# Optimization experiments

Measured on AMD Instinct MI355X. Metric: run time of the kernel, lower is better.

Reference implementation:

```python
import jax, jax.numpy as jnp
import numpy as np

NUM_HEADS = 8
AGENT_NUM = 144
POOL_SIZE = 12  # int(sqrt(agent_num))


def _adaptive_pool_matrix(H, out):
    # Row i averages input rows [floor(i*H/out), ceil((i+1)*H/out)) -- PyTorch AdaptiveAvgPool2d semantics.
    P = np.zeros((out, H), dtype=np.float32)
    for i in range(out):
        s = (i * H) // out
        e = -((-(i + 1) * H) // out)
        P[i, s:e] = 1.0 / (e - s)
    return jnp.asarray(P)


def setup_inputs() -> dict:
    key = jax.random.key(0)
    ks = jax.random.split(key, 4)
    b, n, c = 16, 3136, 512
    return {
        "x": jax.random.normal(ks[0], (b, n, c), dtype=jnp.float32),
        "qkv_w": jax.random.normal(ks[1], (3 * c, c), dtype=jnp.float32) * 0.02,
        "proj_w": jax.random.normal(ks[2], (c, c), dtype=jnp.float32) * 0.02,
        "proj_b": jnp.zeros((c,), dtype=jnp.float32),
        "dwc_w": jax.random.normal(ks[3], (c, 1, 3, 3), dtype=jnp.float32) * 0.1,
        "dwc_b": jnp.zeros((c,), dtype=jnp.float32),
    }


def reference(x, qkv_w, proj_w, proj_b, dwc_w, dwc_b):
    b, n, c = x.shape
    H = NUM_HEADS
    d = c // H
    hh = int(n ** 0.5)  # 56
    scale = d ** -0.5

    qkv = x @ qkv_w.T  # (b, n, 3c)
    q, k, v = jnp.split(qkv, 3, axis=-1)

    # adaptive avg pool of q (as b,h,w,c image) down to 12x12 -> agent tokens
    P = _adaptive_pool_matrix(hh, POOL_SIZE)  # (12, 56)
    agent = jnp.einsum('ph,qw,bhwc->bpqc', P, P, q.reshape(b, hh, hh, c))
    agent = agent.reshape(b, AGENT_NUM, c)

    def heads(t):
        return t.reshape(b, -1, H, d).transpose(0, 2, 1, 3)  # (b, H, L, d)

    qh, kh, vh, ah = heads(q), heads(k), heads(v), heads(agent)

    # stage 1: agent-to-key attention
    agent_attn = jax.nn.softmax((ah * scale) @ kh.transpose(0, 1, 3, 2), axis=-1)  # (b,H,144,n)
    agent_v = agent_attn @ vh  # (b,H,144,d)

    # stage 2: query-to-agent attention
    q_attn = jax.nn.softmax((qh * scale) @ ah.transpose(0, 1, 3, 2), axis=-1)  # (b,H,n,144)
    out = (q_attn @ agent_v).transpose(0, 2, 1, 3).reshape(b, n, c)

    # depthwise 3x3 conv residual on v image
    v_img = v.reshape(b, hh, hh, c).transpose(0, 3, 1, 2)  # NCHW
    dw = jax.lax.conv_general_dilated(
        v_img, dwc_w, window_strides=(1, 1), padding='SAME',
        feature_group_count=c, dimension_numbers=('NCHW', 'OIHW', 'NCHW'))
    dw = dw + dwc_b[None, :, None, None]
    out = out + dw.transpose(0, 2, 3, 1).reshape(b, n, c)

    return out @ proj_w.T + proj_b
```

## Files before the change

kernel.cpp:

```cpp
#include <hip/hip_runtime.h>
#include <hip/hip_bf16.h>
#include <math.h>

typedef unsigned short u16;
typedef __attribute__((ext_vector_type(8))) unsigned short u16x8;
typedef __attribute__((ext_vector_type(8))) short bf16x8;
typedef __attribute__((ext_vector_type(4))) float f32x4;

#define BATCH 16
#define NTOK  3136
#define CHN   512
#define NH    8
#define HD    64
#define HHW   56
#define NAG   144
#define PS    12

#define S1PP   72
#define S2PP   152
#define ASP    72
#define AVP    152

__device__ __forceinline__ float b2f(u16 u) {
    unsigned int x = ((unsigned int)u) << 16;
    float f;
    __builtin_memcpy(&f, &x, 4);
    return f;
}
__device__ __forceinline__ u16 f2b(float f) {
    unsigned int x;
    __builtin_memcpy(&x, &f, 4);
    unsigned int lsb = (x >> 16) & 1u;
    x += 0x7fffu + lsb;
    return (u16)(x >> 16);
}
__device__ __forceinline__ void store1(float* p, float v) { *p = v; }
__device__ __forceinline__ void store1(u16* p, float v)   { *p = f2b(v); }

__global__ __launch_bounds__(256) void cvt_f32_bf16_kernel(
    const float* __restrict__ src, u16* __restrict__ dst, int n4)
{
    const int idx = blockIdx.x * 256 + threadIdx.x;
    if (idx >= n4) return;
    float4 v = reinterpret_cast<const float4*>(src)[idx];
    ushort4 o;
    o.x = f2b(v.x); o.y = f2b(v.y); o.z = f2b(v.z); o.w = f2b(v.w);
    reinterpret_cast<ushort4*>(dst)[idx] = o;
}

template <typename OT, bool BIAS>
__global__ __launch_bounds__(256) void mfma_gemm_kernel(
    const u16* __restrict__ A, const u16* __restrict__ W,
    const float* __restrict__ bias, OT* __restrict__ out)
{
    __shared__ u16 Asm[128 * 64];
    __shared__ u16 Bsm[128 * 64];

    const int tid  = threadIdx.x;
    const int lane = tid & 63;
    const int w    = tid >> 6;
    const int m0   = blockIdx.x * 128;
    const int n0   = blockIdx.y * 128;
    const int wm   = (w & 1) * 64;
    const int wn   = (w >> 1) * 64;

    const int srow = lane >> 3;
    const int scol = (lane & 7) * 8;

    f32x4 acc[4][4] = {};

    for (int kt = 0; kt < 8; ++kt) {
        const int k0 = kt * 64;
        __syncthreads();
        #pragma unroll
        for (int i = 0; i < 4; ++i) {
            const int rb = w * 8 + i * 32;
            __builtin_amdgcn_global_load_lds(
                (const __attribute__((address_space(1))) void*)
                    (A + (size_t)(m0 + rb + srow) * 512 + k0 + scol),
                (__attribute__((address_space(3))) void*)(Asm + rb * 64),
                16, 0, 0);
        }
        #pragma unroll
        for (int i = 0; i < 4; ++i) {
            const int rb = w * 8 + i * 32;
            __builtin_amdgcn_global_load_lds(
                (const __attribute__((address_space(1))) void*)
                    (W + (size_t)(n0 + rb + srow) * 512 + k0 + scol),
                (__attribute__((address_space(3))) void*)(Bsm + rb * 64),
                16, 0, 0);
        }
        __syncthreads();

        #pragma unroll
        for (int kh = 0; kh < 2; ++kh) {
            bf16x8 af[4], bfr[4];
            #pragma unroll
            for (int t = 0; t < 4; ++t)
                af[t] = *reinterpret_cast<const bf16x8*>(
                    &Asm[(wm + t * 16 + (lane & 15)) * 64 + kh * 32 + (lane >> 4) * 8]);
            #pragma unroll
            for (int t = 0; t < 4; ++t)
                bfr[t] = *reinterpret_cast<const bf16x8*>(
                    &Bsm[(wn + t * 16 + (lane & 15)) * 64 + kh * 32 + (lane >> 4) * 8]);
            #pragma unroll
            for (int i = 0; i < 4; ++i)
                #pragma unroll
                for (int j = 0; j < 4; ++j)
                    acc[i][j] = __builtin_amdgcn_mfma_f32_16x16x32_bf16(
                        af[i], bfr[j], acc[i][j], 0, 0, 0);
        }
    }

    const int quad = lane >> 4;
    const int col  = lane & 15;
    #pragma unroll
    for (int j = 0; j < 4; ++j) {
        const int n = n0 + wn + j * 16 + col;
        const float bv = BIAS ? bias[n] : 0.f;
        #pragma unroll
        for (int i = 0; i < 4; ++i) {
            #pragma unroll
            for (int r = 0; r < 4; ++r) {
                const int m = m0 + wm + i * 16 + quad * 4 + r;
                store1(&out[(size_t)m * 512 + n], acc[i][j][r] + bv);
            }
        }
    }
}

__global__ __launch_bounds__(256) void pool_x_kernel(
    const float* __restrict__ x, u16* __restrict__ x_pool)
{
    const int b = blockIdx.x, pq = blockIdx.y;
    const int p = pq / PS, qq = pq % PS;
    const int sp_ = (p * HHW) / PS, ep_ = ((p + 1) * HHW + PS - 1) / PS;
    const int sq_ = (qq * HHW) / PS, eq_ = ((qq + 1) * HHW + PS - 1) / PS;
    const float inv = 1.0f / (float)((ep_ - sp_) * (eq_ - sq_));
    for (int ch = threadIdx.x; ch < CHN; ch += 256) {
        float acc = 0.f;
        for (int y = sp_; y < ep_; ++y)
            for (int xx = sq_; xx < eq_; ++xx)
                acc += x[((size_t)b * NTOK + y * HHW + xx) * CHN + ch];
        x_pool[((size_t)b * NAG + pq) * CHN + ch] = f2b(acc * inv);
    }
}

__global__ __launch_bounds__(256) void transpose_v_kernel(
    const u16* __restrict__ v, u16* __restrict__ vt)
{
    __shared__ u16 T[64 * S1PP + 32];
    const int t0 = blockIdx.x * 64;
    const int c0 = blockIdx.y * 64;
    const int b  = blockIdx.z;

    const int r  = threadIdx.x >> 2;
    const int cc = (threadIdx.x & 3) * 16;
    const u16* src = v + ((size_t)b * NTOK + t0 + r) * CHN + c0 + cc;
    u16x8 a0 = *reinterpret_cast<const u16x8*>(src);
    u16x8 a1 = *reinterpret_cast<const u16x8*>(src + 8);
    const int skw = (cc >> 4) * 8;
    #pragma unroll
    for (int j = 0; j < 8; ++j) T[(cc + j) * S1PP + r + skw] = a0[j];
    #pragma unroll
    for (int j = 0; j < 8; ++j) T[(cc + 8 + j) * S1PP + r + skw] = a1[j];
    __syncthreads();

    const int cr  = threadIdx.x >> 2;
    const int tt  = (threadIdx.x & 3) * 16;
    const int rsk = (cr >> 4) * 8;
    u16* dst = vt + ((size_t)b * CHN + c0 + cr) * NTOK + t0 + tt;
    *reinterpret_cast<u16x8*>(dst)     = *reinterpret_cast<const u16x8*>(&T[cr * S1PP + tt + rsk]);
    *reinterpret_cast<u16x8*>(dst + 8) = *reinterpret_cast<const u16x8*>(&T[cr * S1PP + tt + 8 + rsk]);
}

__global__ __launch_bounds__(64) void stage1_mfma_kernel(
    const u16* __restrict__ k, const u16* __restrict__ vt,
    const u16* __restrict__ agent, u16* __restrict__ avt)
{
    __shared__ u16 Pl[16 * S1PP];

    const int lb   = blockIdx.x;
    const int work = (lb & 7) * 144 + (lb >> 3);
    const int at   = work % 9;
    const int r2   = work / 9;
    const int h    = r2 & 7;
    const int b    = r2 >> 3;

    const int lane = threadIdx.x;
    const int c = lane & 15, g = lane >> 4;

    const u16* kp = k  + (size_t)b * NTOK * CHN + h * HD;
    const u16* vp = vt + ((size_t)(b * NH + h)) * HD * NTOK;
    const u16* ap = agent + ((size_t)b * NAG + at * 16 + c) * CHN + h * HD + g * 8;

    bf16x8 af0 = *reinterpret_cast<const bf16x8*>(ap);
    bf16x8 af1 = *reinterpret_cast<const bf16x8*>(ap + 32);

    f32x4 accO[4] = {};
    float m_ = -1e30f, l_ = 0.f;

    bf16x8 kf[8];
    #pragma unroll
    for (int kt = 0; kt < 4; ++kt)
        #pragma unroll
        for (int ks = 0; ks < 2; ++ks)
            kf[kt * 2 + ks] = *reinterpret_cast<const bf16x8*>(
                kp + (size_t)(kt * 16 + c) * CHN + ks * 32 + g * 8);

    for (int key0 = 0; key0 < NTOK; key0 += 64) {
        bf16x8 vf[8];
        #pragma unroll
        for (int dt = 0; dt < 4; ++dt)
            #pragma unroll
            for (int kk = 0; kk < 2; ++kk)
                vf[dt * 2 + kk] = *reinterpret_cast<const bf16x8*>(
                    vp + (size_t)(dt * 16 + c) * NTOK + key0 + kk * 32 + g * 8);
        bf16x8 kn[8];
        const bool more = (key0 + 64) < NTOK;
        if (more) {
            #pragma unroll
            for (int kt = 0; kt < 4; ++kt)
                #pragma unroll
                for (int ks = 0; ks < 2; ++ks)
                    kn[kt * 2 + ks] = *reinterpret_cast<const bf16x8*>(
                        kp + (size_t)(key0 + 64 + kt * 16 + c) * CHN + ks * 32 + g * 8);
        }

        f32x4 s[4] = {};
        #pragma unroll
        for (int kt = 0; kt < 4; ++kt) {
            s[kt] = __builtin_amdgcn_mfma_f32_16x16x32_bf16(kf[kt * 2 + 0], af0, s[kt], 0, 0, 0);
            s[kt] = __builtin_amdgcn_mfma_f32_16x16x32_bf16(kf[kt * 2 + 1], af1, s[kt], 0, 0, 0);
        }

        float tmax = -1e30f;
        #pragma unroll
        for (int kt = 0; kt < 4; ++kt)
            #pragma unroll
            for (int r = 0; r < 4; ++r) tmax = fmaxf(tmax, s[kt][r]);
        tmax = fmaxf(tmax, __shfl_xor(tmax, 16));
        tmax = fmaxf(tmax, __shfl_xor(tmax, 32));

        const float mnew  = fmaxf(m_, tmax * 0.125f);
        const float alpha = __expf(m_ - mnew);
        float psum = 0.f;
        #pragma unroll
        for (int kt = 0; kt < 4; ++kt) {
            float p0 = __expf(s[kt][0] * 0.125f - mnew);
            float p1 = __expf(s[kt][1] * 0.125f - mnew);
            float p2 = __expf(s[kt][2] * 0.125f - mnew);
            float p3 = __expf(s[kt][3] * 0.125f - mnew);
            psum += (p0 + p1) + (p2 + p3);
            ushort4 pk;
            pk.x = f2b(p0); pk.y = f2b(p1); pk.z = f2b(p2); pk.w = f2b(p3);
            *reinterpret_cast<ushort4*>(&Pl[c * S1PP + kt * 16 + g * 4]) = pk;
        }
        psum += __shfl_xor(psum, 16);
        psum += __shfl_xor(psum, 32);
        l_ = l_ * alpha + psum;
        m_ = mnew;
        #pragma unroll
        for (int dt = 0; dt < 4; ++dt) {
            accO[dt][0] *= alpha; accO[dt][1] *= alpha;
            accO[dt][2] *= alpha; accO[dt][3] *= alpha;
        }

        asm volatile("s_waitcnt lgkmcnt(0)" ::: "memory");
        __builtin_amdgcn_sched_barrier(0);

        bf16x8 pf0 = *reinterpret_cast<const bf16x8*>(&Pl[c * S1PP + g * 8]);
        bf16x8 pf1 = *reinterpret_cast<const bf16x8*>(&Pl[c * S1PP + 32 + g * 8]);

        #pragma unroll
        for (int dt = 0; dt < 4; ++dt) {
            accO[dt] = __builtin_amdgcn_mfma_f32_16x16x32_bf16(vf[dt * 2 + 0], pf0, accO[dt], 0, 0, 0);
            accO[dt] = __builtin_amdgcn_mfma_f32_16x16x32_bf16(vf[dt * 2 + 1], pf1, accO[dt], 0, 0, 0);
        }

        if (more) {
            #pragma unroll
            for (int i = 0; i < 8; ++i) kf[i] = kn[i];
        }
    }

    const float invl = 1.f / l_;
    const size_t dbase = (size_t)(b * NH + h) * HD;
    #pragma unroll
    for (int dt = 0; dt < 4; ++dt)
        #pragma unroll
        for (int r = 0; r < 4; ++r)
            avt[(dbase + dt * 16 + g * 4 + r) * NAG + at * 16 + c] =
                f2b(accO[dt][r] * invl);
}

__global__ __launch_bounds__(256, 3) void stage2_mfma_kernel(
    const u16* __restrict__ q,
    const u16* __restrict__ agent,
    const u16* __restrict__ avt,
    const u16* __restrict__ v,
    const float* __restrict__ dwc_w,
    const float* __restrict__ dwc_b,
    u16* __restrict__ xattn)
{
    __shared__ __align__(16) u16 AsPl[NAG * ASP];
    __shared__ __align__(16) u16 AVs[HD * AVP];
    __shared__ float dwW[HD * 9];
    __shared__ float dwB[HD];

    const int h   = blockIdx.y;
    const int b   = blockIdx.z;
    const int tid = threadIdx.x;
    const int w    = tid >> 6;
    const int lane = tid & 63;
    const int c = lane & 15, g = lane >> 4;
    const int q0 = (blockIdx.x * 4 + w) * 16;
    const int qg = q0 + c;
    const int y = qg / HHW, xx = qg % HHW;

    const u16* qp = q + ((size_t)b * NTOK + qg) * CHN + h * HD + g * 8;
    bf16x8 qf0 = *reinterpret_cast<const bf16x8*>(qp);
    bf16x8 qf1 = *reinterpret_cast<const bf16x8*>(qp + 32);

    {
        const u16* ab = agent + (size_t)b * NAG * CHN + h * HD;
        for (int idx = tid; idx < NAG * 4; idx += 256) {
            const int r = idx >> 2, cc = (idx & 3) * 16;
            *reinterpret_cast<u16x8*>(&AsPl[r * ASP + cc]) =
                *reinterpret_cast<const u16x8*>(ab + (size_t)r * CHN + cc);
            *reinterpret_cast<u16x8*>(&AsPl[r * ASP + cc + 8]) =
                *reinterpret_cast<const u16x8*>(ab + (size_t)r * CHN + cc + 8);
        }
        const u16* avb = avt + (size_t)(b * NH + h) * HD * NAG;
        for (int idx = tid; idx < HD * 18; idx += 256) {
            const int r = idx / 18, cc = (idx % 18) * 8;
            *reinterpret_cast<u16x8*>(&AVs[r * AVP + cc]) =
                *reinterpret_cast<const u16x8*>(avb + (size_t)r * NAG + cc);
        }
        for (int idx = tid; idx < HD * 9; idx += 256)
            dwW[idx] = dwc_w[(h * HD + idx / 9) * 9 + (idx % 9)];
        if (tid < HD) dwB[tid] = dwc_b[h * HD + tid];
    }
    __syncthreads();

    float conv[4][4];
    #pragma unroll
    for (int dt = 0; dt < 4; ++dt)
        #pragma unroll
        for (int r = 0; r < 4; ++r) conv[dt][r] = 0.f;
    {
        const u16* vq = v + ((size_t)b * NTOK + qg) * CHN + h * HD + g * 4;
        #pragma unroll
        for (int dy = -1; dy <= 1; ++dy) {
            #pragma unroll
            for (int dx = -1; dx <= 1; ++dx) {
                const int tap = (dy + 1) * 3 + (dx + 1);
                const int yy = y + dy, xc = xx + dx;
                const bool ok = (yy >= 0 && yy < HHW && xc >= 0 && xc < HHW);
                const u16* vr = vq + (ok ? (ptrdiff_t)(dy * HHW + dx) * CHN : 0);
                ushort4 vv0 = *reinterpret_cast<const ushort4*>(vr);
                ushort4 vv1 = *reinterpret_cast<const ushort4*>(vr + 16);
                ushort4 vv2 = *reinterpret_cast<const ushort4*>(vr + 32);
                ushort4 vv3 = *reinterpret_cast<const ushort4*>(vr + 48);
                if (ok) {
                    const float* wt = &dwW[(g * 4) * 9 + tap];
                    conv[0][0] += b2f(vv0.x) * wt[(0 * 16 + 0) * 9];
                    conv[0][1] += b2f(vv0.y) * wt[(0 * 16 + 1) * 9];
                    conv[0][2] += b2f(vv0.z) * wt[(0 * 16 + 2) * 9];
                    conv[0][3] += b2f(vv0.w) * wt[(0 * 16 + 3) * 9];
                    conv[1][0] += b2f(vv1.x) * wt[(1 * 16 + 0) * 9];
                    conv[1][1] += b2f(vv1.y) * wt[(1 * 16 + 1) * 9];
                    conv[1][2] += b2f(vv1.z) * wt[(1 * 16 + 2) * 9];
                    conv[1][3] += b2f(vv1.w) * wt[(1 * 16 + 3) * 9];
                    conv[2][0] += b2f(vv2.x) * wt[(2 * 16 + 0) * 9];
                    conv[2][1] += b2f(vv2.y) * wt[(2 * 16 + 1) * 9];
                    conv[2][2] += b2f(vv2.z) * wt[(2 * 16 + 2) * 9];
                    conv[2][3] += b2f(vv2.w) * wt[(2 * 16 + 3) * 9];
                    conv[3][0] += b2f(vv3.x) * wt[(3 * 16 + 0) * 9];
                    conv[3][1] += b2f(vv3.y) * wt[(3 * 16 + 1) * 9];
                    conv[3][2] += b2f(vv3.z) * wt[(3 * 16 + 2) * 9];
                    conv[3][3] += b2f(vv3.w) * wt[(3 * 16 + 3) * 9];
                }
            }
        }
    }

    f32x4 s[9] = {};
    #pragma unroll
    for (int t = 0; t < 9; ++t) {
        bf16x8 af0 = *reinterpret_cast<const bf16x8*>(&AsPl[(t * 16 + c) * ASP + g * 8]);
        bf16x8 af1 = *reinterpret_cast<const bf16x8*>(&AsPl[(t * 16 + c) * ASP + 32 + g * 8]);
        s[t] = __builtin_amdgcn_mfma_f32_16x16x32_bf16(af0, qf0, s[t], 0, 0, 0);
        s[t] = __builtin_amdgcn_mfma_f32_16x16x32_bf16(af1, qf1, s[t], 0, 0, 0);
    }

    __syncthreads();

    float mx = -1e30f;
    #pragma unroll
    for (int t = 0; t < 9; ++t)
        #pragma unroll
        for (int r = 0; r < 4; ++r) mx = fmaxf(mx, s[t][r]);
    mx = fmaxf(mx, __shfl_xor(mx, 16));
    mx = fmaxf(mx, __shfl_xor(mx, 32));
    mx *= 0.125f;

    u16* Pw = &AsPl[w * 16 * S2PP];
    float ls = 0.f;
    #pragma unroll
    for (int t = 0; t < 9; ++t) {
        float p0 = __expf(s[t][0] * 0.125f - mx);
        float p1 = __expf(s[t][1] * 0.125f - mx);
        float p2 = __expf(s[t][2] * 0.125f - mx);
        float p3 = __expf(s[t][3] * 0.125f - mx);
        ls += (p0 + p1) + (p2 + p3);
        ushort4 pk;
        pk.x = f2b(p0); pk.y = f2b(p1); pk.z = f2b(p2); pk.w = f2b(p3);
        *reinterpret_cast<ushort4*>(&Pw[c * S2PP + t * 16 + g * 4]) = pk;
    }
    ls += __shfl_xor(ls, 16);
    ls += __shfl_xor(ls, 32);
    const float inv = 1.f / ls;

    asm volatile("s_waitcnt lgkmcnt(0)" ::: "memory");
    __builtin_amdgcn_sched_barrier(0);

    f32x4 o[4] = {};
    #pragma unroll
    for (int sl = 0; sl < 4; ++sl) {
        bf16x8 pf = *reinterpret_cast<const bf16x8*>(&Pw[c * S2PP + sl * 32 + g * 8]);
        #pragma unroll
        for (int dt = 0; dt < 4; ++dt) {
            bf16x8 avf = *reinterpret_cast<const bf16x8*>(
                &AVs[(dt * 16 + c) * AVP + sl * 32 + g * 8]);
            o[dt] = __builtin_amdgcn_mfma_f32_16x16x32_bf16(avf, pf, o[dt], 0, 0, 0);
        }
    }
    {
        bf16x8 pf = {};
        bf16x8 avf[4] = {{0,0,0,0,0,0,0,0},{0,0,0,0,0,0,0,0},
                         {0,0,0,0,0,0,0,0},{0,0,0,0,0,0,0,0}};
        if (g < 2) {
            pf = *reinterpret_cast<const bf16x8*>(&Pw[c * S2PP + 128 + g * 8]);
            #pragma unroll
            for (int dt = 0; dt < 4; ++dt)
                avf[dt] = *reinterpret_cast<const bf16x8*>(
                    &AVs[(dt * 16 + c) * AVP + 128 + g * 8]);
        }
        #pragma unroll
        for (int dt = 0; dt < 4; ++dt)
            o[dt] = __builtin_amdgcn_mfma_f32_16x16x32_bf16(avf[dt], pf, o[dt], 0, 0, 0);
    }

    u16* outp = xattn + ((size_t)b * NTOK + qg) * CHN + h * HD + g * 4;
    #pragma unroll
    for (int dt = 0; dt < 4; ++dt) {
        ushort4 o4;
        o4.x = f2b(o[dt][0] * inv + dwB[dt * 16 + g * 4 + 0] + conv[dt][0]);
        o4.y = f2b(o[dt][1] * inv + dwB[dt * 16 + g * 4 + 1] + conv[dt][1]);
        o4.z = f2b(o[dt][2] * inv + dwB[dt * 16 + g * 4 + 2] + conv[dt][2]);
        o4.w = f2b(o[dt][3] * inv + dwB[dt * 16 + g * 4 + 3] + conv[dt][3]);
        *reinterpret_cast<ushort4*>(outp + dt * 16) = o4;
    }
}

extern "C" void kernel_launch(void* const* d_in, const int* in_sizes, int n_in,
                              void* d_out, int out_size, void* d_ws, size_t ws_size,
                              hipStream_t stream)
{
    const float* x      = (const float*)d_in[0];
    const float* qkv_w  = (const float*)d_in[1];
    const float* proj_w = (const float*)d_in[2];
    const float* proj_b = (const float*)d_in[3];
    const float* dwc_w  = (const float*)d_in[4];
    const float* dwc_b  = (const float*)d_in[5];
    float* out = (float*)d_out;

    const size_t nqkv = (size_t)BATCH * NTOK * CHN;
    u16* xb  = (u16*)d_out;
    u16* vt  = xb + nqkv;
    u16* qb  = xb + nqkv;
    u16* kb  = (u16*)d_in[0];
    u16* vb  = kb + nqkv;
    u16* attn = kb;

    char* p = (char*)d_ws;
    u16* x_pool  = (u16*)p;  p += (size_t)BATCH * NAG * CHN * 2;
    u16* agent   = (u16*)p;  p += (size_t)BATCH * NAG * CHN * 2;
    u16* avt     = (u16*)p;  p += (size_t)BATCH * NH * HD * NAG * 2;
    u16* wb      = (u16*)p;
    u16* Wq_b = wb;
    u16* Wk_b = wb + (size_t)262144;
    u16* Wv_b = wb + (size_t)524288;
    u16* Wp_b = wb + (size_t)786432;

    pool_x_kernel<<<dim3(BATCH, NAG), 256, 0, stream>>>(x, x_pool);
    cvt_f32_bf16_kernel<<<(int)(nqkv / 4 + 255) / 256, 256, 0, stream>>>(x, xb, (int)(nqkv / 4));
    cvt_f32_bf16_kernel<<<(786432 / 4 + 255) / 256, 256, 0, stream>>>(qkv_w, wb, 786432 / 4);
    cvt_f32_bf16_kernel<<<(262144 / 4 + 255) / 256, 256, 0, stream>>>(proj_w, Wp_b, 262144 / 4);
    mfma_gemm_kernel<u16, false><<<dim3(18, 4), 256, 0, stream>>>(x_pool, Wq_b, nullptr, agent);
    mfma_gemm_kernel<u16, false><<<dim3(392, 4), 256, 0, stream>>>(xb, Wk_b, nullptr, kb);
    mfma_gemm_kernel<u16, false><<<dim3(392, 4), 256, 0, stream>>>(xb, Wv_b, nullptr, vb);
    transpose_v_kernel<<<dim3(NTOK / 64, CHN / 64, BATCH), 256, 0, stream>>>(vb, vt);
    stage1_mfma_kernel<<<dim3(1152), 64, 0, stream>>>(kb, vt, agent, avt);
    mfma_gemm_kernel<u16, false><<<dim3(392, 4), 256, 0, stream>>>(xb, Wq_b, nullptr, qb);
    stage2_mfma_kernel<<<dim3(49, NH, BATCH), 256, 0, stream>>>(
        qb, agent, avt, vb, dwc_w, dwc_b, attn);
    mfma_gemm_kernel<float, true><<<dim3(392, 4), 256, 0, stream>>>(attn, Wp_b, proj_b, out);
}
```

Measured before the change: 728.6 us.

## Fuse V transpose into V-projection GEMM epilogue and remap workgroups for XCD locality

The V projection GEMM now writes a transposed copy of its output through shared memory in the epilogue, removing the separate transpose kernel and its extra global read of V. All GEMM launches also remap linear block ids so that blocks dispatched to the same XCD cover contiguous tiles, aiming at better L2 reuse. The fused epilogue adds LDS traffic, a larger shared buffer and extra syncs to one GEMM, which may reduce its occupancy.

```diff
diff --git a/kernel.cpp b/kernel.cpp
--- a/kernel.cpp
+++ b/kernel.cpp
@@ -20,6 +20,7 @@
 #define S2PP   152
 #define ASP    72
 #define AVP    152
+#define TRP    136
 
 __device__ __forceinline__ float b2f(u16 u) {
     unsigned int x = ((unsigned int)u) << 16;
@@ -48,19 +49,30 @@
     reinterpret_cast<ushort4*>(dst)[idx] = o;
 }
 
-template <typename OT, bool BIAS>
+template <typename OT, bool BIAS, bool TRB>
 __global__ __launch_bounds__(256) void mfma_gemm_kernel(
     const u16* __restrict__ A, const u16* __restrict__ W,
-    const float* __restrict__ bias, OT* __restrict__ out)
+    const float* __restrict__ bias, OT* __restrict__ out,
+    u16* __restrict__ vt_out)
 {
-    __shared__ u16 Asm[128 * 64];
-    __shared__ u16 Bsm[128 * 64];
+    __shared__ u16 SH[TRB ? 128 * TRP : 16384];
+    u16* Asm = SH;
+    u16* Bsm = SH + 8192;
 
     const int tid  = threadIdx.x;
     const int lane = tid & 63;
     const int w    = tid >> 6;
-    const int m0   = blockIdx.x * 128;
-    const int n0   = blockIdx.y * 128;
+
+    const int nwg = gridDim.x * gridDim.y;
+    const int lid = blockIdx.y * gridDim.x + blockIdx.x;
+    int wid = lid;
+    if ((nwg & 7) == 0) {
+        const int chunk = nwg >> 3;
+        wid = (lid & 7) * chunk + (lid >> 3);
+    }
+    const int m0 = (wid >> 2) * 128;
+    const int n0 = (wid & 3) * 128;
+
     const int wm   = (w & 1) * 64;
     const int wn   = (w >> 1) * 64;
 
@@ -125,6 +137,34 @@
                 const int m = m0 + wm + i * 16 + quad * 4 + r;
                 store1(&out[(size_t)m * 512 + n], acc[i][j][r] + bv);
             }
+        }
+    }
+
+    if constexpr (TRB) {
+        __syncthreads();
+        #pragma unroll
+        for (int j = 0; j < 4; ++j) {
+            const int nl = wn + j * 16 + col;
+            #pragma unroll
+            for (int i = 0; i < 4; ++i)
+                #pragma unroll
+                for (int r = 0; r < 4; ++r) {
+                    const int ml = wm + i * 16 + quad * 4 + r;
+                    SH[nl * TRP + ml] = f2b(acc[i][j][r]);
+                }
+        }
+        __syncthreads();
+        const int nr = tid >> 1, mh = (tid & 1) * 64;
+        const int ng = n0 + nr;
+        #pragma unroll
+        for (int kc = 0; kc < 8; ++kc) {
+            const int ml  = mh + kc * 8;
+            const int gm  = m0 + ml;
+            const int bb  = gm / NTOK;
+            const int tok = gm - bb * NTOK;
+            u16x8 val = *reinterpret_cast<const u16x8*>(&SH[nr * TRP + ml]);
+            *reinterpret_cast<u16x8*>(
+                &vt_out[((size_t)bb * CHN + ng) * NTOK + tok]) = val;
         }
     }
 }
@@ -144,34 +184,6 @@
                 acc += x[((size_t)b * NTOK + y * HHW + xx) * CHN + ch];
         x_pool[((size_t)b * NAG + pq) * CHN + ch] = f2b(acc * inv);
     }
-}
-
-__global__ __launch_bounds__(256) void transpose_v_kernel(
-    const u16* __restrict__ v, u16* __restrict__ vt)
-{
-    __shared__ u16 T[64 * S1PP + 32];
-    const int t0 = blockIdx.x * 64;
-    const int c0 = blockIdx.y * 64;
-    const int b  = blockIdx.z;
-
-    const int r  = threadIdx.x >> 2;
-    const int cc = (threadIdx.x & 3) * 16;
-    const u16* src = v + ((size_t)b * NTOK + t0 + r) * CHN + c0 + cc;
-    u16x8 a0 = *reinterpret_cast<const u16x8*>(src);
-    u16x8 a1 = *reinterpret_cast<const u16x8*>(src + 8);
-    const int skw = (cc >> 4) * 8;
-    #pragma unroll
-    for (int j = 0; j < 8; ++j) T[(cc + j) * S1PP + r + skw] = a0[j];
-    #pragma unroll
-    for (int j = 0; j < 8; ++j) T[(cc + 8 + j) * S1PP + r + skw] = a1[j];
-    __syncthreads();
-
-    const int cr  = threadIdx.x >> 2;
-    const int tt  = (threadIdx.x & 3) * 16;
-    const int rsk = (cr >> 4) * 8;
-    u16* dst = vt + ((size_t)b * CHN + c0 + cr) * NTOK + t0 + tt;
-    *reinterpret_cast<u16x8*>(dst)     = *reinterpret_cast<const u16x8*>(&T[cr * S1PP + tt + rsk]);
-    *reinterpret_cast<u16x8*>(dst + 8) = *reinterpret_cast<const u16x8*>(&T[cr * S1PP + tt + 8 + rsk]);
 }
 
 __global__ __launch_bounds__(64) void stage1_mfma_kernel(
@@ -498,13 +510,17 @@
     cvt_f32_bf16_kernel<<<(int)(nqkv / 4 + 255) / 256, 256, 0, stream>>>(x, xb, (int)(nqkv / 4));
     cvt_f32_bf16_kernel<<<(786432 / 4 + 255) / 256, 256, 0, stream>>>(qkv_w, wb, 786432 / 4);
     cvt_f32_bf16_kernel<<<(262144 / 4 + 255) / 256, 256, 0, stream>>>(proj_w, Wp_b, 262144 / 4);
-    mfma_gemm_kernel<u16, false><<<dim3(18, 4), 256, 0, stream>>>(x_pool, Wq_b, nullptr, agent);
-    mfma_gemm_kernel<u16, false><<<dim3(392, 4), 256, 0, stream>>>(xb, Wk_b, nullptr, kb);
-    mfma_gemm_kernel<u16, false><<<dim3(392, 4), 256, 0, stream>>>(xb, Wv_b, nullptr, vb);
-    transpose_v_kernel<<<dim3(NTOK / 64, CHN / 64, BATCH), 256, 0, stream>>>(vb, vt);
+    mfma_gemm_kernel<u16, false, false><<<dim3(18, 4), 256, 0, stream>>>(
+        x_pool, Wq_b, nullptr, agent, nullptr);
+    mfma_gemm_kernel<u16, false, false><<<dim3(392, 4), 256, 0, stream>>>(
+        xb, Wk_b, nullptr, kb, nullptr);
+    mfma_gemm_kernel<u16, false, true><<<dim3(392, 4), 256, 0, stream>>>(
+        xb, Wv_b, nullptr, vb, vt);
     stage1_mfma_kernel<<<dim3(1152), 64, 0, stream>>>(kb, vt, agent, avt);
-    mfma_gemm_kernel<u16, false><<<dim3(392, 4), 256, 0, stream>>>(xb, Wq_b, nullptr, qb);
+    mfma_gemm_kernel<u16, false, false><<<dim3(392, 4), 256, 0, stream>>>(
+        xb, Wq_b, nullptr, qb, nullptr);
     stage2_mfma_kernel<<<dim3(49, NH, BATCH), 256, 0, stream>>>(
         qb, agent, avt, vb, dwc_w, dwc_b, attn);
-    mfma_gemm_kernel<float, true><<<dim3(392, 4), 256, 0, stream>>>(attn, Wp_b, proj_b, out);
-}
+    mfma_gemm_kernel<float, true, false><<<dim3(392, 4), 256, 0, stream>>>(
+        attn, Wp_b, proj_b, out, nullptr);
+}
```

New measurement: 711.4 us. 2.4% less time.
